# Optimization experiments

Measured on AMD Instinct MI355X. Metric: run time of the kernel, lower is better.

The kernel has to match this reference:

```python
import jax, jax.numpy as jnp
import numpy as np

C = 384      # c_s
NF = 16      # n_freq
H = 256      # mlp_hidden
B, K, N = 4, 2048, 16384
POS_WEIGHT = 1.5  # not used; see below


def _ln(x, g, b, eps=1e-5):
    m = x.mean(-1, keepdims=True)
    v = ((x - m) ** 2).mean(-1, keepdims=True)
    return (x - m) * jax.lax.rsqrt(v + eps) * g + b


def setup_inputs() -> dict:
    key = jax.random.key(0)
    ks = jax.random.split(key, 24)
    w = lambda k, shp: (jax.random.normal(k, shp, jnp.float32) * 0.02)
    inp = {
        "s_parent": jax.random.normal(ks[0], (B, K, C), jnp.float32),
        "mu_k": jax.random.normal(ks[1], (B, K, 3), jnp.float32),
        "R_k": jax.random.normal(ks[2], (B, K, 3, 3), jnp.float32),
        "s_k": jax.random.uniform(ks[3], (B, K, 3), jnp.float32),
        "a_idx": jax.random.randint(ks[4], (B, N), 0, K, jnp.int32),
        "node_mask": jnp.ones((B, N), jnp.float32),
        "pos01": jax.random.uniform(ks[5], (B, N), jnp.float32),
        # Pos01FourierEncoder: Linear(2*NF -> C)
        "pos_w": w(ks[6], (C, 2 * NF)), "pos_b": jnp.zeros((C,), jnp.float32),
        # q_proj: LayerNorm(C), Linear(C,C), SiLU, Linear(C,C)
        "q_ln_g": jnp.ones((C,), jnp.float32), "q_ln_b": jnp.zeros((C,), jnp.float32),
        "q_w1": w(ks[7], (C, C)), "q_b1": jnp.zeros((C,), jnp.float32),
        "q_w2": w(ks[8], (C, C)), "q_b2": jnp.zeros((C,), jnp.float32),
        # mlp: LayerNorm(C), Linear(C,H), SiLU, Linear(H,H), SiLU, Linear(H,3)
        "m_ln_g": jnp.ones((C,), jnp.float32), "m_ln_b": jnp.zeros((C,), jnp.float32),
        "m_w1": w(ks[9], (H, C)), "m_b1": jnp.zeros((H,), jnp.float32),
        "m_w2": w(ks[10], (H, H)), "m_b2": jnp.zeros((H,), jnp.float32),
        "m_w3": w(ks[11], (3, H)), "m_b3": jnp.zeros((3,), jnp.float32),
    }
    return inp


def reference(s_parent, mu_k, R_k, s_k, a_idx, node_mask, pos01,
              pos_w, pos_b, q_ln_g, q_ln_b, q_w1, q_b1, q_w2, q_b2,
              m_ln_g, m_ln_b, m_w1, m_b1, m_w2, m_b2, m_w3, m_b3):
    pos_weight = 1.0
    scale = 1.5
    mask = node_mask[..., None]  # [B,N,1]

    # Fourier positional encoding of pos01 in [0,1]
    freqs = (2.0 ** jnp.arange(NF, dtype=jnp.float32)) * np.float32(np.pi)
    ang = pos01[..., None] * freqs                          # [B,N,NF]
    feats = jnp.concatenate([jnp.sin(ang), jnp.cos(ang)], -1)  # [B,N,2NF]
    pos_emb = (feats @ pos_w.T + pos_b) * mask              # [B,N,C]

    idx = jnp.clip(a_idx, 0, K - 1)
    s_pi = jnp.take_along_axis(s_parent, idx[:, :, None], axis=1)  # [B,N,C]
    s_pi = s_pi + pos_weight * pos_emb

    # q_proj
    q = _ln(s_pi, q_ln_g, q_ln_b)
    q = jax.nn.silu(q @ q_w1.T + q_b1)
    q = (q @ q_w2.T + q_b2) * mask

    # mlp -> xi_hat
    h = _ln(q, m_ln_g, m_ln_b)
    h = jax.nn.silu(h @ m_w1.T + m_b1)
    h = jax.nn.silu(h @ m_w2.T + m_b2)
    xi = (h @ m_w3.T + m_b3) * mask
    xi_hat = jnp.tanh(xi) * scale                           # [B,N,3]

    # gather parent rigid params per node
    mu_i = jnp.take_along_axis(mu_k, idx[:, :, None], axis=1)            # [B,N,3]
    s_i = jnp.take_along_axis(jnp.maximum(s_k, 1e-8), idx[:, :, None], axis=1)
    R_i = jnp.take_along_axis(R_k, idx[:, :, None, None], axis=1)        # [B,N,3,3]

    # rigid apply: x = R @ (xi * s) + mu
    x_hat = jnp.einsum('bnij,bnj->bni', R_i, xi_hat * s_i) + mu_i
    x_hat = x_hat * mask
    return xi_hat, x_hat * 10.0, pos01
```

## Files before the change

kernel.cpp:

```cpp
#include <hip/hip_runtime.h>
#include <hip/hip_bf16.h>
#include <math.h>

#define C 384
#define NF 16
#define H 256
#define Bb 4
#define Kk 2048
#define Nn 16384
#define MB 64
#define LDA 392

typedef __attribute__((ext_vector_type(8))) short bf16x8;
typedef __attribute__((ext_vector_type(4))) float f32x4;
typedef __attribute__((ext_vector_type(4))) short s16x4;

#define POS_OFF 0
#define Q1_OFF  12288
#define Q2_OFF  159744
#define M1_OFF  307200
#define M2_OFF  405504
#define M3_OFF  471040
#define W_TOTAL 475136
#define GQ_OFF 0
#define CQ_OFF 384
#define GM_OFF 768
#define CM_OFF 1024

__device__ __attribute__((always_inline)) inline short f2bf(float x) {
    return __builtin_bit_cast(short, __float2bfloat16(x));
}
__device__ __attribute__((always_inline)) inline float bf2f(short s) {
    return __bfloat162float(__builtin_bit_cast(__hip_bfloat16, s));
}
__device__ __attribute__((always_inline)) inline float silu(float v) {
    return v * __builtin_amdgcn_rcpf(1.f + __expf(-v));
}

__global__ __launch_bounds__(256) void conv_w(
    const float* __restrict__ pos_w, const float* __restrict__ q_w1,
    const float* __restrict__ q_w2,  const float* __restrict__ m_w1,
    const float* __restrict__ m_w2,  const float* __restrict__ m_w3,
    const float* __restrict__ q_ln_g, const float* __restrict__ m_ln_g,
    short* __restrict__ ws)
{
    int i = blockIdx.x * 256 + threadIdx.x;
    if (i >= W_TOTAL) return;
    const float* src; int off, K;
    if      (i < Q1_OFF) { src = pos_w; off = POS_OFF; K = 32; }
    else if (i < Q2_OFF) { src = q_w1;  off = Q1_OFF;  K = 384; }
    else if (i < M1_OFF) { src = q_w2;  off = Q2_OFF;  K = 384; }
    else if (i < M2_OFF) { src = m_w1;  off = M1_OFF;  K = 384; }
    else if (i < M3_OFF) { src = m_w2;  off = M2_OFF;  K = 256; }
    else                 { src = m_w3;  off = M3_OFF;  K = 256; }
    int t = i - off;
    int chunk = t >> 9, r = t & 511;
    int ln = r >> 5, kq = r & 31;
    int NKm = K >> 5;
    int ntg = chunk / NKm, kk = chunk - ntg * NKm;
    int f = ntg * 16 + ln, k = kk * 32 + kq;
    float v;
    if (off == M3_OFF) v = (f < 3) ? m_w3[f * 256 + k] : 0.f;
    else               v = src[(size_t)f * K + k];
    if (off == Q1_OFF) v *= q_ln_g[k];
    if (off == M1_OFF) v *= m_ln_g[k];
    ws[i] = f2bf(v);
}

__global__ __launch_bounds__(256) void fold_consts(
    const float* __restrict__ q_w1, const float* __restrict__ q_b1,
    const float* __restrict__ q_ln_g, const float* __restrict__ q_ln_b,
    const float* __restrict__ m_w1, const float* __restrict__ m_b1,
    const float* __restrict__ m_ln_g, const float* __restrict__ m_ln_b,
    float* __restrict__ cst)
{
    int f = blockIdx.x * 256 + threadIdx.x;
    if (f < 384) {
        float g = 0.f, c = 0.f;
        for (int k = 0; k < 384; ++k) {
            float w = q_w1[(size_t)f * 384 + k];
            g += bf2f(f2bf(w * q_ln_g[k]));
            c += w * q_ln_b[k];
        }
        cst[GQ_OFF + f] = g;
        cst[CQ_OFF + f] = c + q_b1[f];
    } else if (f < 640) {
        int f2 = f - 384;
        float g = 0.f, c = 0.f;
        for (int k = 0; k < 384; ++k) {
            float w = m_w1[(size_t)f2 * 384 + k];
            g += bf2f(f2bf(w * m_ln_g[k]));
            c += w * m_ln_b[k];
        }
        cst[GM_OFF + f2] = g;
        cst[CM_OFF + f2] = c + m_b1[f2];
    }
}

template<int K, int NT, int NTN, int KN, bool SILU_, bool MASK, bool LNIN, bool STATS>
__device__ __attribute__((always_inline)) inline void layer_ip(
    const short* __restrict__ W, const float* __restrict__ cb,
    const float* __restrict__ Gf, int FB,
    const short* __restrict__ Wn, int FBn,
    bf16x8 (&bin)[6],
    short (*__restrict__ xs)[LDA],
    float (*__restrict__ sc1)[4], float (*__restrict__ sc2)[4],
    const float* __restrict__ wmask, int w, int q, int ln)
{
    constexpr int NK = K / 32;
    const short* bp[NT];
    #pragma unroll
    for (int nt = 0; nt < NT; ++nt)
        bp[nt] = W + ((size_t)(FB / 16 + nt) * NK) * 512 + ln * 32 + q * 8;

    f32x4 acc[4][NT];
    #pragma unroll
    for (int mt = 0; mt < 4; ++mt)
        #pragma unroll
        for (int nt = 0; nt < NT; ++nt)
            acc[mt][nt] = (f32x4){0.f, 0.f, 0.f, 0.f};

    bf16x8 b0[NT], b1[NT], a0[4], a1[4];
    #pragma unroll
    for (int nt = 0; nt < NT; ++nt) b0[nt] = bin[nt];
    #pragma unroll
    for (int mt = 0; mt < 4; ++mt) a0[mt] = *(const bf16x8*)&xs[mt * 16 + ln][q * 8];

    #pragma unroll
    for (int kc = 0; kc < NK; kc += 2) {
        #pragma unroll
        for (int nt = 0; nt < NT; ++nt) b1[nt] = *(const bf16x8*)(bp[nt] + (kc + 1) * 512);
        #pragma unroll
        for (int mt = 0; mt < 4; ++mt) a1[mt] = *(const bf16x8*)&xs[mt * 16 + ln][(kc + 1) * 32 + q * 8];
        #pragma unroll
        for (int nt = 0; nt < NT; ++nt)
            #pragma unroll
            for (int mt = 0; mt < 4; ++mt)
                acc[mt][nt] = __builtin_amdgcn_mfma_f32_16x16x32_bf16(b0[nt], a0[mt], acc[mt][nt], 0, 0, 0);
        if (kc + 2 < NK) {
            #pragma unroll
            for (int nt = 0; nt < NT; ++nt) b0[nt] = *(const bf16x8*)(bp[nt] + (kc + 2) * 512);
            #pragma unroll
            for (int mt = 0; mt < 4; ++mt) a0[mt] = *(const bf16x8*)&xs[mt * 16 + ln][(kc + 2) * 32 + q * 8];
        }
        #pragma unroll
        for (int nt = 0; nt < NT; ++nt)
            #pragma unroll
            for (int mt = 0; mt < 4; ++mt)
                acc[mt][nt] = __builtin_amdgcn_mfma_f32_16x16x32_bf16(b1[nt], a1[mt], acc[mt][nt], 0, 0, 0);
    }

    #pragma unroll
    for (int nt = 0; nt < NTN; ++nt)
        bin[nt] = *(const bf16x8*)(Wn + ((size_t)(FBn / 16 + nt) * (KN / 32)) * 512 + ln * 32 + q * 8);

    __syncthreads();

    float mk[4], rstd[4], rm[4];
    #pragma unroll
    for (int mt = 0; mt < 4; ++mt) {
        int m = mt * 16 + ln;
        if (MASK) mk[mt] = wmask[m];
        if (LNIN) {
            f32x4 p1 = *(const f32x4*)&sc1[m][0];
            f32x4 p2 = *(const f32x4*)&sc2[m][0];
            float t1 = p1[0] + p1[1] + p1[2] + p1[3];
            float t2 = p2[0] + p2[1] + p2[2] + p2[3];
            float mean = t1 * (1.f / 384.f);
            float var  = t2 * (1.f / 384.f) - mean * mean;
            rstd[mt] = rsqrtf(var + 1e-5f);
            rm[mt]   = rstd[mt] * mean;
        }
    }

    float s1[4] = {0.f,0.f,0.f,0.f}, s2[4] = {0.f,0.f,0.f,0.f};
    #pragma unroll
    for (int nt = 0; nt < NT; ++nt) {
        const int f0 = FB + nt * 16 + q * 4;
        f32x4 c4 = *(const f32x4*)&cb[f0];
        f32x4 g4;
        if (LNIN) g4 = *(const f32x4*)&Gf[f0];
        #pragma unroll
        for (int mt = 0; mt < 4; ++mt) {
            s16x4 o4;
            #pragma unroll
            for (int r = 0; r < 4; ++r) {
                float v;
                if (LNIN) v = fmaf(rstd[mt], acc[mt][nt][r], fmaf(-rm[mt], g4[r], c4[r]));
                else      v = acc[mt][nt][r] + c4[r];
                if (SILU_) v = silu(v);
                if (MASK) v *= mk[mt];
                if (STATS) { s1[mt] += v; s2[mt] += v * v; }
                o4[r] = f2bf(v);
            }
            *(s16x4*)&xs[mt * 16 + ln][f0] = o4;
        }
    }
    if (STATS) {
        #pragma unroll
        for (int mt = 0; mt < 4; ++mt) {
            s1[mt] += __shfl_xor(s1[mt], 16); s2[mt] += __shfl_xor(s2[mt], 16);
            s1[mt] += __shfl_xor(s1[mt], 32); s2[mt] += __shfl_xor(s2[mt], 32);
        }
        if (q == 0) {
            #pragma unroll
            for (int mt = 0; mt < 4; ++mt) {
                sc1[mt * 16 + ln][w] = s1[mt];
                sc2[mt * 16 + ln][w] = s2[mt];
            }
        }
    }
    __syncthreads();
}

__global__ __launch_bounds__(256, 2) void upxi64(
    const float* __restrict__ s_parent, const float* __restrict__ mu_k,
    const float* __restrict__ R_k,      const float* __restrict__ s_k,
    const int*   __restrict__ a_idx,    const float* __restrict__ node_mask,
    const float* __restrict__ pos01,
    const float* __restrict__ pos_b,
    const float* __restrict__ q_b2,     const float* __restrict__ m_b2,
    const float* __restrict__ m_b3,
    const short* __restrict__ wsb,      const float* __restrict__ cst,
    float* __restrict__ out)
{
    __shared__ short xs[MB][LDA];
    __shared__ float sc1[MB][4];
    __shared__ float sc2[MB][4];
    __shared__ float wmask[MB], wpos[MB];
    __shared__ int   widx[MB];

    const int tid  = threadIdx.x;
    const int w    = tid >> 6;
    const int lane = tid & 63;
    const int q    = lane >> 4;
    const int ln   = lane & 15;

    const int g0 = blockIdx.x * MB;
    const int b  = g0 / Nn;
    const int n0 = g0 % Nn;

    bf16x8 bin[6];
    #pragma unroll
    for (int nt = 0; nt < 6; ++nt)
        bin[nt] = *(const bf16x8*)(wsb + Q1_OFF + ((size_t)(w * 6 + nt) * 12) * 512 + ln * 32 + q * 8);

    if (tid < MB) {
        int gi = b * Nn + n0 + tid;
        int idx = a_idx[gi];
        widx[tid]  = min(max(idx, 0), Kk - 1);
        wmask[tid] = node_mask[gi];
        wpos[tid]  = pos01[gi];
    }
    __syncthreads();

    const float* gbase = s_parent + (long)b * Kk * C;

    {
        const short* pos_wb = wsb + POS_OFF;
        const bool use_sin = (q < 2);
        const int kb = (q & 1) * 8;
        bf16x8 a[4];
        #pragma unroll
        for (int mt = 0; mt < 4; ++mt) {
            float p = wpos[mt * 16 + ln];
            #pragma unroll
            for (int e = 0; e < 8; ++e) {
                float fr = (float)(1 << (kb + e)) * 3.14159265358979323846f;
                float sv, cv;
                __sincosf(p * fr, &sv, &cv);
                a[mt][e] = f2bf(use_sin ? sv : cv);
            }
        }
        f32x4 acc[4][6];
        #pragma unroll
        for (int mt = 0; mt < 4; ++mt)
            #pragma unroll
            for (int nt = 0; nt < 6; ++nt)
                acc[mt][nt] = (f32x4){0.f, 0.f, 0.f, 0.f};
        #pragma unroll
        for (int nt = 0; nt < 6; ++nt) {
            bf16x8 bfr = *(const bf16x8*)&pos_wb[(w * 6 + nt) * 512 + ln * 32 + q * 8];
            #pragma unroll
            for (int mt = 0; mt < 4; ++mt)
                acc[mt][nt] = __builtin_amdgcn_mfma_f32_16x16x32_bf16(bfr, a[mt], acc[mt][nt], 0, 0, 0);
        }
        float mk[4]; int ix[4];
        #pragma unroll
        for (int mt = 0; mt < 4; ++mt) {
            mk[mt] = wmask[mt * 16 + ln];
            ix[mt] = widx[mt * 16 + ln];
        }
        float s1[4] = {0.f,0.f,0.f,0.f}, s2[4] = {0.f,0.f,0.f,0.f};
        #pragma unroll
        for (int nt = 0; nt < 6; ++nt) {
            const int f0 = w * 96 + nt * 16 + q * 4;
            f32x4 pb4 = *(const f32x4*)&pos_b[f0];
            #pragma unroll
            for (int mt = 0; mt < 4; ++mt) {
                f32x4 g4 = *(const f32x4*)&gbase[(long)ix[mt] * C + f0];
                s16x4 o4;
                #pragma unroll
                for (int r = 0; r < 4; ++r) {
                    float v = (acc[mt][nt][r] + pb4[r]) * mk[mt] + g4[r];
                    s1[mt] += v; s2[mt] += v * v;
                    o4[r] = f2bf(v);
                }
                *(s16x4*)&xs[mt * 16 + ln][f0] = o4;
            }
        }
        #pragma unroll
        for (int mt = 0; mt < 4; ++mt) {
            s1[mt] += __shfl_xor(s1[mt], 16); s2[mt] += __shfl_xor(s2[mt], 16);
            s1[mt] += __shfl_xor(s1[mt], 32); s2[mt] += __shfl_xor(s2[mt], 32);
        }
        if (q == 0) {
            #pragma unroll
            for (int mt = 0; mt < 4; ++mt) {
                sc1[mt * 16 + ln][w] = s1[mt];
                sc2[mt * 16 + ln][w] = s2[mt];
            }
        }
    }
    __syncthreads();

    layer_ip<384, 6, 6, 384, true,  false, true,  false>(wsb + Q1_OFF, cst + CQ_OFF,
        cst + GQ_OFF, w * 96, wsb + Q2_OFF, w * 96, bin, xs, sc1, sc2, wmask, w, q, ln);
    layer_ip<384, 6, 4, 384, false, true,  false, true >(wsb + Q2_OFF, q_b2,
        nullptr, w * 96, wsb + M1_OFF, w * 64, bin, xs, sc1, sc2, wmask, w, q, ln);
    layer_ip<384, 4, 4, 256, true,  false, true,  false>(wsb + M1_OFF, cst + CM_OFF,
        cst + GM_OFF, w * 64, wsb + M2_OFF, w * 64, bin, xs, sc1, sc2, wmask, w, q, ln);
    layer_ip<256, 4, 1, 256, true,  false, false, false>(wsb + M2_OFF, m_b2,
        nullptr, w * 64, wsb + M3_OFF, 0, bin, xs, sc1, sc2, wmask, w, q, ln);

    {
        const short* W3 = wsb + M3_OFF;
        f32x4 a3 = (f32x4){0.f, 0.f, 0.f, 0.f};
        #pragma unroll
        for (int kc = 0; kc < 8; ++kc) {
            bf16x8 a  = *(const bf16x8*)&xs[w * 16 + ln][kc * 32 + q * 8];
            bf16x8 bf = (kc == 0) ? bin[0]
                      : *(const bf16x8*)(W3 + kc * 512 + ln * 32 + q * 8);
            a3 = __builtin_amdgcn_mfma_f32_16x16x32_bf16(bf, a, a3, 0, 0, 0);
        }
        if (q == 0) {
            int m = w * 16 + ln;
            float mkv = wmask[m];
            #pragma unroll
            for (int r = 0; r < 3; ++r) {
                float v = (a3[r] + m_b3[r]) * mkv;
                sc1[m][r] = tanhf(v) * 1.5f;
            }
        }
    }

    if (lane < 16) {
        int m = w * 16 + lane;
        long gi = (long)b * Nn + n0 + m;
        long pk = (long)b * Kk + widx[m];
        float mkv = wmask[m];
        float xv[3], yv[3], xiv[3];
        #pragma unroll
        for (int j = 0; j < 3; ++j) {
            xiv[j] = sc1[m][j];
            float sc = fmaxf(s_k[pk * 3 + j], 1e-8f);
            xv[j] = xiv[j] * sc;
        }
        #pragma unroll
        for (int i = 0; i < 3; ++i) {
            float a = R_k[pk * 9 + i * 3 + 0] * xv[0]
                    + R_k[pk * 9 + i * 3 + 1] * xv[1]
                    + R_k[pk * 9 + i * 3 + 2] * xv[2]
                    + mu_k[pk * 3 + i];
            yv[i] = a * mkv * 10.f;
        }
        float* o0 = out;
        float* o1 = out + (long)Bb * Nn * 3;
        float* o2 = out + (long)Bb * Nn * 6;
        #pragma unroll
        for (int j = 0; j < 3; ++j) { o0[gi * 3 + j] = xiv[j]; o1[gi * 3 + j] = yv[j]; }
        o2[gi] = wpos[m];
    }
}

extern "C" void kernel_launch(void* const* d_in, const int* in_sizes, int n_in,
                              void* d_out, int out_size, void* d_ws, size_t ws_size,
                              hipStream_t stream) {
    const float* s_parent = (const float*)d_in[0];
    const float* mu_k     = (const float*)d_in[1];
    const float* R_k      = (const float*)d_in[2];
    const float* s_k      = (const float*)d_in[3];
    const int*   a_idx    = (const int*)  d_in[4];
    const float* node_mask= (const float*)d_in[5];
    const float* pos01    = (const float*)d_in[6];
    const float* pos_w    = (const float*)d_in[7];
    const float* pos_b    = (const float*)d_in[8];
    const float* q_ln_g   = (const float*)d_in[9];
    const float* q_ln_b   = (const float*)d_in[10];
    const float* q_w1     = (const float*)d_in[11];
    const float* q_b1     = (const float*)d_in[12];
    const float* q_w2     = (const float*)d_in[13];
    const float* q_b2     = (const float*)d_in[14];
    const float* m_ln_g   = (const float*)d_in[15];
    const float* m_ln_b   = (const float*)d_in[16];
    const float* m_w1     = (const float*)d_in[17];
    const float* m_b1     = (const float*)d_in[18];
    const float* m_w2     = (const float*)d_in[19];
    const float* m_b2     = (const float*)d_in[20];
    const float* m_w3     = (const float*)d_in[21];
    const float* m_b3     = (const float*)d_in[22];

    short* wsb = (short*)d_ws;
    float* cst = (float*)(wsb + W_TOTAL);

    conv_w<<<(W_TOTAL + 255) / 256, 256, 0, stream>>>(
        pos_w, q_w1, q_w2, m_w1, m_w2, m_w3, q_ln_g, m_ln_g, wsb);
    fold_consts<<<3, 256, 0, stream>>>(
        q_w1, q_b1, q_ln_g, q_ln_b, m_w1, m_b1, m_ln_g, m_ln_b, cst);

    int blocks = (Bb * Nn) / MB;
    upxi64<<<blocks, 256, 0, stream>>>(
        s_parent, mu_k, R_k, s_k, a_idx, node_mask, pos01,
        pos_b, q_b2, m_b2, m_b3, wsb, cst, (float*)d_out);
}
```

Measured before the change: 208.0 us.

## Halve rows per block to 32, raise occupancy, merge prep kernels

The main kernel now processes 32 rows per block instead of 64. This halves accumulator and A-fragment registers, and the launch bound rises to 3 blocks per SM. The two weight-prep kernels are merged into one launch, with the constant folding parallelised as one block per output feature and a wave-shuffle reduction. Bf16 conversion now packs pairs. The trade is that each weight fragment is reused across fewer rows, so weight traffic per row doubles, and half the waves sit idle in the final 3-output layer.

```diff
diff --git a/kernel.cpp b/kernel.cpp
--- a/kernel.cpp
+++ b/kernel.cpp
@@ -8,7 +8,7 @@
 #define Bb 4
 #define Kk 2048
 #define Nn 16384
-#define MB 64
+#define MB 32
 #define LDA 392
 
 typedef __attribute__((ext_vector_type(8))) short bf16x8;
@@ -22,6 +22,7 @@
 #define M2_OFF  405504
 #define M3_OFF  471040
 #define W_TOTAL 475136
+#define NCONV   ((W_TOTAL + 255) / 256)
 #define GQ_OFF 0
 #define CQ_OFF 384
 #define GM_OFF 768
@@ -36,64 +37,70 @@
 __device__ __attribute__((always_inline)) inline float silu(float v) {
     return v * __builtin_amdgcn_rcpf(1.f + __expf(-v));
 }
-
-__global__ __launch_bounds__(256) void conv_w(
+__device__ __attribute__((always_inline)) inline s16x4 pack4(f32x4 v) {
+    __hip_bfloat162 p0 = __float22bfloat162_rn(float2{v[0], v[1]});
+    __hip_bfloat162 p1 = __float22bfloat162_rn(float2{v[2], v[3]});
+    s16x4 o;
+    o[0] = __builtin_bit_cast(short, p0.x);
+    o[1] = __builtin_bit_cast(short, p0.y);
+    o[2] = __builtin_bit_cast(short, p1.x);
+    o[3] = __builtin_bit_cast(short, p1.y);
+    return o;
+}
+
+__global__ __launch_bounds__(256) void prep(
     const float* __restrict__ pos_w, const float* __restrict__ q_w1,
     const float* __restrict__ q_w2,  const float* __restrict__ m_w1,
     const float* __restrict__ m_w2,  const float* __restrict__ m_w3,
-    const float* __restrict__ q_ln_g, const float* __restrict__ m_ln_g,
-    short* __restrict__ ws)
+    const float* __restrict__ q_ln_g, const float* __restrict__ q_ln_b,
+    const float* __restrict__ m_ln_g, const float* __restrict__ m_ln_b,
+    const float* __restrict__ q_b1,   const float* __restrict__ m_b1,
+    short* __restrict__ ws, float* __restrict__ cst)
 {
-    int i = blockIdx.x * 256 + threadIdx.x;
-    if (i >= W_TOTAL) return;
-    const float* src; int off, K;
-    if      (i < Q1_OFF) { src = pos_w; off = POS_OFF; K = 32; }
-    else if (i < Q2_OFF) { src = q_w1;  off = Q1_OFF;  K = 384; }
-    else if (i < M1_OFF) { src = q_w2;  off = Q2_OFF;  K = 384; }
-    else if (i < M2_OFF) { src = m_w1;  off = M1_OFF;  K = 384; }
-    else if (i < M3_OFF) { src = m_w2;  off = M2_OFF;  K = 256; }
-    else                 { src = m_w3;  off = M3_OFF;  K = 256; }
-    int t = i - off;
-    int chunk = t >> 9, r = t & 511;
-    int ln = r >> 5, kq = r & 31;
-    int NKm = K >> 5;
-    int ntg = chunk / NKm, kk = chunk - ntg * NKm;
-    int f = ntg * 16 + ln, k = kk * 32 + kq;
-    float v;
-    if (off == M3_OFF) v = (f < 3) ? m_w3[f * 256 + k] : 0.f;
-    else               v = src[(size_t)f * K + k];
-    if (off == Q1_OFF) v *= q_ln_g[k];
-    if (off == M1_OFF) v *= m_ln_g[k];
-    ws[i] = f2bf(v);
-}
-
-__global__ __launch_bounds__(256) void fold_consts(
-    const float* __restrict__ q_w1, const float* __restrict__ q_b1,
-    const float* __restrict__ q_ln_g, const float* __restrict__ q_ln_b,
-    const float* __restrict__ m_w1, const float* __restrict__ m_b1,
-    const float* __restrict__ m_ln_g, const float* __restrict__ m_ln_b,
-    float* __restrict__ cst)
-{
-    int f = blockIdx.x * 256 + threadIdx.x;
-    if (f < 384) {
-        float g = 0.f, c = 0.f;
-        for (int k = 0; k < 384; ++k) {
-            float w = q_w1[(size_t)f * 384 + k];
-            g += bf2f(f2bf(w * q_ln_g[k]));
-            c += w * q_ln_b[k];
-        }
-        cst[GQ_OFF + f] = g;
-        cst[CQ_OFF + f] = c + q_b1[f];
-    } else if (f < 640) {
-        int f2 = f - 384;
-        float g = 0.f, c = 0.f;
-        for (int k = 0; k < 384; ++k) {
-            float w = m_w1[(size_t)f2 * 384 + k];
-            g += bf2f(f2bf(w * m_ln_g[k]));
-            c += w * m_ln_b[k];
-        }
-        cst[GM_OFF + f2] = g;
-        cst[CM_OFF + f2] = c + m_b1[f2];
+    __shared__ float rg[4], rc[4];
+    int tid = threadIdx.x;
+    int blk = blockIdx.x;
+    if (blk < NCONV) {
+        int i = blk * 256 + tid;
+        if (i >= W_TOTAL) return;
+        const float* src; int off, K;
+        if      (i < Q1_OFF) { src = pos_w; off = POS_OFF; K = 32; }
+        else if (i < Q2_OFF) { src = q_w1;  off = Q1_OFF;  K = 384; }
+        else if (i < M1_OFF) { src = q_w2;  off = Q2_OFF;  K = 384; }
+        else if (i < M2_OFF) { src = m_w1;  off = M1_OFF;  K = 384; }
+        else if (i < M3_OFF) { src = m_w2;  off = M2_OFF;  K = 256; }
+        else                 { src = m_w3;  off = M3_OFF;  K = 256; }
+        int t = i - off;
+        int chunk = t >> 9, r = t & 511;
+        int ln = r >> 5, kq = r & 31;
+        int NKm = K >> 5;
+        int ntg = chunk / NKm, kk = chunk - ntg * NKm;
+        int f = ntg * 16 + ln, k = kk * 32 + kq;
+        float v;
+        if (off == M3_OFF) v = (f < 3) ? m_w3[f * 256 + k] : 0.f;
+        else               v = src[(size_t)f * K + k];
+        if (off == Q1_OFF) v *= q_ln_g[k];
+        if (off == M1_OFF) v *= m_ln_g[k];
+        ws[i] = f2bf(v);
+        return;
+    }
+    int f = blk - NCONV;
+    const float *Wsrc, *lng, *lnb, *bias; int fr, go, co;
+    if (f < 384) { Wsrc = q_w1; lng = q_ln_g; lnb = q_ln_b; bias = q_b1; fr = f;      go = GQ_OFF; co = CQ_OFF; }
+    else         { Wsrc = m_w1; lng = m_ln_g; lnb = m_ln_b; bias = m_b1; fr = f - 384; go = GM_OFF; co = CM_OFF; }
+    float g = 0.f, c = 0.f;
+    for (int k = tid; k < 384; k += 256) {
+        float wv = Wsrc[(size_t)fr * 384 + k];
+        g += bf2f(f2bf(wv * lng[k]));
+        c += wv * lnb[k];
+    }
+    #pragma unroll
+    for (int d = 1; d < 64; d <<= 1) { g += __shfl_xor(g, d); c += __shfl_xor(c, d); }
+    if ((tid & 63) == 0) { rg[tid >> 6] = g; rc[tid >> 6] = c; }
+    __syncthreads();
+    if (tid == 0) {
+        cst[go + fr] = rg[0] + rg[1] + rg[2] + rg[3];
+        cst[co + fr] = rc[0] + rc[1] + rc[2] + rc[3] + bias[fr];
     }
 }
 
@@ -113,40 +120,40 @@
     for (int nt = 0; nt < NT; ++nt)
         bp[nt] = W + ((size_t)(FB / 16 + nt) * NK) * 512 + ln * 32 + q * 8;
 
-    f32x4 acc[4][NT];
-    #pragma unroll
-    for (int mt = 0; mt < 4; ++mt)
+    f32x4 acc[2][NT];
+    #pragma unroll
+    for (int mt = 0; mt < 2; ++mt)
         #pragma unroll
         for (int nt = 0; nt < NT; ++nt)
             acc[mt][nt] = (f32x4){0.f, 0.f, 0.f, 0.f};
 
-    bf16x8 b0[NT], b1[NT], a0[4], a1[4];
+    bf16x8 b0[NT], b1[NT], a0[2], a1[2];
     #pragma unroll
     for (int nt = 0; nt < NT; ++nt) b0[nt] = bin[nt];
     #pragma unroll
-    for (int mt = 0; mt < 4; ++mt) a0[mt] = *(const bf16x8*)&xs[mt * 16 + ln][q * 8];
+    for (int mt = 0; mt < 2; ++mt) a0[mt] = *(const bf16x8*)&xs[mt * 16 + ln][q * 8];
 
     #pragma unroll
     for (int kc = 0; kc < NK; kc += 2) {
         #pragma unroll
         for (int nt = 0; nt < NT; ++nt) b1[nt] = *(const bf16x8*)(bp[nt] + (kc + 1) * 512);
         #pragma unroll
-        for (int mt = 0; mt < 4; ++mt) a1[mt] = *(const bf16x8*)&xs[mt * 16 + ln][(kc + 1) * 32 + q * 8];
+        for (int mt = 0; mt < 2; ++mt) a1[mt] = *(const bf16x8*)&xs[mt * 16 + ln][(kc + 1) * 32 + q * 8];
         #pragma unroll
         for (int nt = 0; nt < NT; ++nt)
             #pragma unroll
-            for (int mt = 0; mt < 4; ++mt)
+            for (int mt = 0; mt < 2; ++mt)
                 acc[mt][nt] = __builtin_amdgcn_mfma_f32_16x16x32_bf16(b0[nt], a0[mt], acc[mt][nt], 0, 0, 0);
         if (kc + 2 < NK) {
             #pragma unroll
             for (int nt = 0; nt < NT; ++nt) b0[nt] = *(const bf16x8*)(bp[nt] + (kc + 2) * 512);
             #pragma unroll
-            for (int mt = 0; mt < 4; ++mt) a0[mt] = *(const bf16x8*)&xs[mt * 16 + ln][(kc + 2) * 32 + q * 8];
+            for (int mt = 0; mt < 2; ++mt) a0[mt] = *(const bf16x8*)&xs[mt * 16 + ln][(kc + 2) * 32 + q * 8];
         }
         #pragma unroll
         for (int nt = 0; nt < NT; ++nt)
             #pragma unroll
-            for (int mt = 0; mt < 4; ++mt)
+            for (int mt = 0; mt < 2; ++mt)
                 acc[mt][nt] = __builtin_amdgcn_mfma_f32_16x16x32_bf16(b1[nt], a1[mt], acc[mt][nt], 0, 0, 0);
     }
 
@@ -156,9 +163,9 @@
 
     __syncthreads();
 
-    float mk[4], rstd[4], rm[4];
-    #pragma unroll
-    for (int mt = 0; mt < 4; ++mt) {
+    float mk[2], rstd[2], rm[2];
+    #pragma unroll
+    for (int mt = 0; mt < 2; ++mt) {
         int m = mt * 16 + ln;
         if (MASK) mk[mt] = wmask[m];
         if (LNIN) {
@@ -173,7 +180,7 @@
         }
     }
 
-    float s1[4] = {0.f,0.f,0.f,0.f}, s2[4] = {0.f,0.f,0.f,0.f};
+    float s1[2] = {0.f, 0.f}, s2[2] = {0.f, 0.f};
     #pragma unroll
     for (int nt = 0; nt < NT; ++nt) {
         const int f0 = FB + nt * 16 + q * 4;
@@ -181,8 +188,8 @@
         f32x4 g4;
         if (LNIN) g4 = *(const f32x4*)&Gf[f0];
         #pragma unroll
-        for (int mt = 0; mt < 4; ++mt) {
-            s16x4 o4;
+        for (int mt = 0; mt < 2; ++mt) {
+            f32x4 vv;
             #pragma unroll
             for (int r = 0; r < 4; ++r) {
                 float v;
@@ -191,20 +198,20 @@
                 if (SILU_) v = silu(v);
                 if (MASK) v *= mk[mt];
                 if (STATS) { s1[mt] += v; s2[mt] += v * v; }
-                o4[r] = f2bf(v);
-            }
-            *(s16x4*)&xs[mt * 16 + ln][f0] = o4;
+                vv[r] = v;
+            }
+            *(s16x4*)&xs[mt * 16 + ln][f0] = pack4(vv);
         }
     }
     if (STATS) {
         #pragma unroll
-        for (int mt = 0; mt < 4; ++mt) {
+        for (int mt = 0; mt < 2; ++mt) {
             s1[mt] += __shfl_xor(s1[mt], 16); s2[mt] += __shfl_xor(s2[mt], 16);
             s1[mt] += __shfl_xor(s1[mt], 32); s2[mt] += __shfl_xor(s2[mt], 32);
         }
         if (q == 0) {
             #pragma unroll
-            for (int mt = 0; mt < 4; ++mt) {
+            for (int mt = 0; mt < 2; ++mt) {
                 sc1[mt * 16 + ln][w] = s1[mt];
                 sc2[mt * 16 + ln][w] = s2[mt];
             }
@@ -213,7 +220,7 @@
     __syncthreads();
 }
 
-__global__ __launch_bounds__(256, 2) void upxi64(
+__global__ __launch_bounds__(256, 3) void upxi32(
     const float* __restrict__ s_parent, const float* __restrict__ mu_k,
     const float* __restrict__ R_k,      const float* __restrict__ s_k,
     const int*   __restrict__ a_idx,    const float* __restrict__ node_mask,
@@ -260,9 +267,9 @@
         const short* pos_wb = wsb + POS_OFF;
         const bool use_sin = (q < 2);
         const int kb = (q & 1) * 8;
-        bf16x8 a[4];
-        #pragma unroll
-        for (int mt = 0; mt < 4; ++mt) {
+        bf16x8 a[2];
+        #pragma unroll
+        for (int mt = 0; mt < 2; ++mt) {
             float p = wpos[mt * 16 + ln];
             #pragma unroll
             for (int e = 0; e < 8; ++e) {
@@ -272,9 +279,9 @@
                 a[mt][e] = f2bf(use_sin ? sv : cv);
             }
         }
-        f32x4 acc[4][6];
-        #pragma unroll
-        for (int mt = 0; mt < 4; ++mt)
+        f32x4 acc[2][6];
+        #pragma unroll
+        for (int mt = 0; mt < 2; ++mt)
             #pragma unroll
             for (int nt = 0; nt < 6; ++nt)
                 acc[mt][nt] = (f32x4){0.f, 0.f, 0.f, 0.f};
@@ -282,41 +289,41 @@
         for (int nt = 0; nt < 6; ++nt) {
             bf16x8 bfr = *(const bf16x8*)&pos_wb[(w * 6 + nt) * 512 + ln * 32 + q * 8];
             #pragma unroll
-            for (int mt = 0; mt < 4; ++mt)
+            for (int mt = 0; mt < 2; ++mt)
                 acc[mt][nt] = __builtin_amdgcn_mfma_f32_16x16x32_bf16(bfr, a[mt], acc[mt][nt], 0, 0, 0);
         }
-        float mk[4]; int ix[4];
-        #pragma unroll
-        for (int mt = 0; mt < 4; ++mt) {
+        float mk[2]; int ix[2];
+        #pragma unroll
+        for (int mt = 0; mt < 2; ++mt) {
             mk[mt] = wmask[mt * 16 + ln];
             ix[mt] = widx[mt * 16 + ln];
         }
-        float s1[4] = {0.f,0.f,0.f,0.f}, s2[4] = {0.f,0.f,0.f,0.f};
+        float s1[2] = {0.f, 0.f}, s2[2] = {0.f, 0.f};
         #pragma unroll
         for (int nt = 0; nt < 6; ++nt) {
             const int f0 = w * 96 + nt * 16 + q * 4;
             f32x4 pb4 = *(const f32x4*)&pos_b[f0];
             #pragma unroll
-            for (int mt = 0; mt < 4; ++mt) {
+            for (int mt = 0; mt < 2; ++mt) {
                 f32x4 g4 = *(const f32x4*)&gbase[(long)ix[mt] * C + f0];
-                s16x4 o4;
+                f32x4 vv;
                 #pragma unroll
                 for (int r = 0; r < 4; ++r) {
                     float v = (acc[mt][nt][r] + pb4[r]) * mk[mt] + g4[r];
                     s1[mt] += v; s2[mt] += v * v;
-                    o4[r] = f2bf(v);
+                    vv[r] = v;
                 }
-                *(s16x4*)&xs[mt * 16 + ln][f0] = o4;
-            }
-        }
-        #pragma unroll
-        for (int mt = 0; mt < 4; ++mt) {
+                *(s16x4*)&xs[mt * 16 + ln][f0] = pack4(vv);
+            }
+        }
+        #pragma unroll
+        for (int mt = 0; mt < 2; ++mt) {
             s1[mt] += __shfl_xor(s1[mt], 16); s2[mt] += __shfl_xor(s2[mt], 16);
             s1[mt] += __shfl_xor(s1[mt], 32); s2[mt] += __shfl_xor(s2[mt], 32);
         }
         if (q == 0) {
             #pragma unroll
-            for (int mt = 0; mt < 4; ++mt) {
+            for (int mt = 0; mt < 2; ++mt) {
                 sc1[mt * 16 + ln][w] = s1[mt];
                 sc2[mt * 16 + ln][w] = s2[mt];
             }
@@ -333,14 +340,13 @@
     layer_ip<256, 4, 1, 256, true,  false, false, false>(wsb + M2_OFF, m_b2,
         nullptr, w * 64, wsb + M3_OFF, 0, bin, xs, sc1, sc2, wmask, w, q, ln);
 
-    {
+    if (w < 2) {
         const short* W3 = wsb + M3_OFF;
         f32x4 a3 = (f32x4){0.f, 0.f, 0.f, 0.f};
         #pragma unroll
         for (int kc = 0; kc < 8; ++kc) {
             bf16x8 a  = *(const bf16x8*)&xs[w * 16 + ln][kc * 32 + q * 8];
-            bf16x8 bf = (kc == 0) ? bin[0]
-                      : *(const bf16x8*)(W3 + kc * 512 + ln * 32 + q * 8);
+            bf16x8 bf = *(const bf16x8*)(W3 + kc * 512 + ln * 32 + q * 8);
             a3 = __builtin_amdgcn_mfma_f32_16x16x32_bf16(bf, a, a3, 0, 0, 0);
         }
         if (q == 0) {
@@ -352,34 +358,33 @@
                 sc1[m][r] = tanhf(v) * 1.5f;
             }
         }
-    }
-
-    if (lane < 16) {
-        int m = w * 16 + lane;
-        long gi = (long)b * Nn + n0 + m;
-        long pk = (long)b * Kk + widx[m];
-        float mkv = wmask[m];
-        float xv[3], yv[3], xiv[3];
-        #pragma unroll
-        for (int j = 0; j < 3; ++j) {
-            xiv[j] = sc1[m][j];
-            float sc = fmaxf(s_k[pk * 3 + j], 1e-8f);
-            xv[j] = xiv[j] * sc;
-        }
-        #pragma unroll
-        for (int i = 0; i < 3; ++i) {
-            float a = R_k[pk * 9 + i * 3 + 0] * xv[0]
-                    + R_k[pk * 9 + i * 3 + 1] * xv[1]
-                    + R_k[pk * 9 + i * 3 + 2] * xv[2]
-                    + mu_k[pk * 3 + i];
-            yv[i] = a * mkv * 10.f;
-        }
-        float* o0 = out;
-        float* o1 = out + (long)Bb * Nn * 3;
-        float* o2 = out + (long)Bb * Nn * 6;
-        #pragma unroll
-        for (int j = 0; j < 3; ++j) { o0[gi * 3 + j] = xiv[j]; o1[gi * 3 + j] = yv[j]; }
-        o2[gi] = wpos[m];
+        if (lane < 16) {
+            int m = w * 16 + lane;
+            long gi = (long)b * Nn + n0 + m;
+            long pk = (long)b * Kk + widx[m];
+            float mkv = wmask[m];
+            float xv[3], yv[3], xiv[3];
+            #pragma unroll
+            for (int j = 0; j < 3; ++j) {
+                xiv[j] = sc1[m][j];
+                float sc = fmaxf(s_k[pk * 3 + j], 1e-8f);
+                xv[j] = xiv[j] * sc;
+            }
+            #pragma unroll
+            for (int i = 0; i < 3; ++i) {
+                float a = R_k[pk * 9 + i * 3 + 0] * xv[0]
+                        + R_k[pk * 9 + i * 3 + 1] * xv[1]
+                        + R_k[pk * 9 + i * 3 + 2] * xv[2]
+                        + mu_k[pk * 3 + i];
+                yv[i] = a * mkv * 10.f;
+            }
+            float* o0 = out;
+            float* o1 = out + (long)Bb * Nn * 3;
+            float* o2 = out + (long)Bb * Nn * 6;
+            #pragma unroll
+            for (int j = 0; j < 3; ++j) { o0[gi * 3 + j] = xiv[j]; o1[gi * 3 + j] = yv[j]; }
+            o2[gi] = wpos[m];
+        }
     }
 }
 
@@ -413,13 +418,12 @@
     short* wsb = (short*)d_ws;
     float* cst = (float*)(wsb + W_TOTAL);
 
-    conv_w<<<(W_TOTAL + 255) / 256, 256, 0, stream>>>(
-        pos_w, q_w1, q_w2, m_w1, m_w2, m_w3, q_ln_g, m_ln_g, wsb);
-    fold_consts<<<3, 256, 0, stream>>>(
-        q_w1, q_b1, q_ln_g, q_ln_b, m_w1, m_b1, m_ln_g, m_ln_b, cst);
+    prep<<<NCONV + 640, 256, 0, stream>>>(
+        pos_w, q_w1, q_w2, m_w1, m_w2, m_w3,
+        q_ln_g, q_ln_b, m_ln_g, m_ln_b, q_b1, m_b1, wsb, cst);
 
     int blocks = (Bb * Nn) / MB;
-    upxi64<<<blocks, 256, 0, stream>>>(
+    upxi32<<<blocks, 256, 0, stream>>>(
         s_parent, mu_k, R_k, s_k, a_idx, node_mask, pos01,
         pos_b, q_b2, m_b2, m_b3, wsb, cst, (float*)d_out);
 }
```

After: 236.1 us. 13.5% more time.
